# Kernel optimization log

Measured on AMD Instinct MI355X. Metric: run time of the kernel, lower is better.

The kernel has to match this reference:

```python
import jax, jax.numpy as jnp
import numpy as np
from math import ceil

WIDTH, HEIGHT, NUM_TILE = 1920, 1080, 16
# NOTE: original code computes BOTH block dims from height (bug preserved for faithfulness)
BLOCK_W = ceil(HEIGHT / NUM_TILE)
BLOCK_H = ceil(HEIGHT / NUM_TILE)
T = NUM_TILE * NUM_TILE  # 256 tiles
N = 65536


def setup_inputs() -> dict:
    key = jax.random.key(0)
    k1, k2, k3 = jax.random.split(key, 3)
    pos2d = jax.random.uniform(k1, (N, 2), jnp.float32) * jnp.array([WIDTH, HEIGHT], jnp.float32)
    radius = jax.random.uniform(k2, (N,), jnp.float32) * 2.0  # radius in tile units, avg ~3x3 tile footprint
    depth = jax.random.uniform(k3, (N,), jnp.float32) * 10.0
    return {"pos2d": pos2d, "radius": radius, "depth": depth}


def _tile_binning(pos2d, radius, depth):
    minval, maxval = 0.0, NUM_TILE - 1e-5
    xmin = jnp.clip(pos2d[:, 0] / BLOCK_W - radius, minval, maxval).astype(jnp.int32)
    xmax = jnp.clip(pos2d[:, 0] / BLOCK_W + radius, minval, maxval).astype(jnp.int32)
    ymin = jnp.clip(pos2d[:, 1] / BLOCK_H - radius, minval, maxval).astype(jnp.int32)
    ymax = jnp.clip(pos2d[:, 1] / BLOCK_H + radius, minval, maxval).astype(jnp.int32)

    tr = jnp.arange(NUM_TILE, dtype=jnp.int32)
    in_x = (tr[None, :] >= xmin[:, None]) & (tr[None, :] <= xmax[:, None])  # [N, 16]
    in_y = (tr[None, :] >= ymin[:, None]) & (tr[None, :] <= ymax[:, None])  # [N, 16]
    # tile index t = xi + NUM_TILE * yi  -> mask[n, yi, xi]
    mask = (in_y[:, :, None] & in_x[:, None, :]).reshape(N, T)  # [N, T]

    # inclusive-cumsum bucket offsets (matches torch.cumsum(tile_count))
    tile_count = jnp.cumsum(mask.sum(axis=0).astype(jnp.int32)).astype(jnp.int32)  # [T]
    total = tile_count[-1]

    # flattened entry list, tile-major then primitive-index order (matches scatter loop order)
    maskT = mask.T.reshape(-1)                                   # [T*N]
    tile_id = jnp.repeat(jnp.arange(T, dtype=jnp.int32), N)      # [T*N]
    prim_id = jnp.tile(jnp.arange(N, dtype=jnp.int32), T)        # [T*N]
    depth_e = depth[prim_id]
    tile_eff = jnp.where(maskT, tile_id, T)  # invalid entries pushed past all real tiles

    # segmented depth sort: primary key tile, secondary depth, tertiary prim (stable tiebreak)
    order = jnp.lexsort((prim_id, depth_e, tile_eff))
    prim_sorted = prim_id[order]
    valid = jnp.arange(T * N) < total
    tile_indices = jnp.where(valid, prim_sorted, -1).astype(jnp.int32)  # [T*N], -1 padded
    return tile_count, tile_indices


def reference(pos2d, radius, depth):
    # Equivalent of Screen.create_tiles(pos2d, radius) followed by Screen.depth_sort(depth).
    # Returns (tile_count: inclusive cumsum bucket offsets [T],
    #          tile_indices: per-tile depth-sorted primitive ids, padded to T*N with -1).
    return _tile_binning(pos2d, radius, depth)
```

## Files before the change

kernel.cpp:

```cpp
#include <hip/hip_runtime.h>
#include <stdint.h>

#define NPRIM 65536
#define NT 16
#define T_TILES 256
#define NBKT 2048
#define BCAP 256
#define NBLK 64
#define CTHR 512

typedef unsigned long long u64;
typedef unsigned int u32;

__device__ __forceinline__ u32 dbucket(float d) {
    u32 b = (u32)(d * 204.8f);
    return b > (NBKT - 1) ? (NBKT - 1) : b;
}

__global__ __launch_bounds__(256) void k_compute(
    const float2* __restrict__ pos2d, const float* __restrict__ radius,
    const float* __restrict__ depth, u64* __restrict__ keysRaw,
    u32* __restrict__ bounds, u32* __restrict__ counts_blk,
    u32* __restrict__ bh)
{
    __shared__ u32 hist[T_TILES];
    __shared__ u32 bhist[NBKT];
    int tid = threadIdx.x;
    hist[tid] = 0;
    for (int j = tid; j < NBKT; j += 256) bhist[j] = 0;
    __syncthreads();

    int base = blockIdx.x * 1024;
    const float mx = (float)(16.0 - 1e-5);
    #pragma unroll
    for (int q = 0; q < 4; ++q) {
        int i = base + q * 256 + tid;
        float2 p = pos2d[i];
        float r = radius[i];
        float fx = p.x / 68.0f;
        float fy = p.y / 68.0f;
        int xmin = (int)fminf(fmaxf(fx - r, 0.0f), mx);
        int xmax = (int)fminf(fmaxf(fx + r, 0.0f), mx);
        int ymin = (int)fminf(fmaxf(fy - r, 0.0f), mx);
        int ymax = (int)fminf(fmaxf(fy + r, 0.0f), mx);
        bounds[i] = (u32)(xmin | (xmax << 4) | (ymin << 8) | (ymax << 12));
        float d = depth[i];
        u32 lrank = atomicAdd(&bhist[dbucket(d)], 1u);
        keysRaw[i] = ((u64)lrank << 48) | ((u64)__float_as_uint(d) << 16) | (u32)i;
        for (int ty = ymin; ty <= ymax; ++ty)
            for (int tx = xmin; tx <= xmax; ++tx)
                atomicAdd(&hist[ty * NT + tx], 1u);
    }
    __syncthreads();
    counts_blk[blockIdx.x * 256 + tid] = hist[tid];
    for (int j = tid; j < NBKT; j += 256) bh[blockIdx.x * NBKT + j] = bhist[j];
}

__global__ __launch_bounds__(256) void k_scatter(
    const u64* __restrict__ keysRaw, const u32* __restrict__ bh,
    u64* __restrict__ keysBkt, u32* __restrict__ bucket_base,
    u32* __restrict__ bucket_count, const u32* __restrict__ counts_blk,
    int* __restrict__ tile_count, u32* __restrict__ excl_off)
{
    __shared__ u32 wsum[4];
    int tid = threadIdx.x, lane = tid & 63, wave = tid >> 6;
    int blk = blockIdx.x;

    if (blk == NBLK) {
        u32 s = 0;
        for (int bb = 0; bb < NBLK; ++bb) s += counts_blk[bb * 256 + tid];
        u32 v = s;
        #pragma unroll
        for (int d = 1; d < 64; d <<= 1) {
            u32 t = __shfl_up(v, d, 64);
            if (lane >= d) v += t;
        }
        if (lane == 63) wsum[wave] = v;
        __syncthreads();
        u32 add = 0;
        for (int w = 0; w < wave; ++w) add += wsum[w];
        u32 incl = v + add;
        tile_count[tid] = (int)incl;
        excl_off[tid] = incl - s;
        return;
    }

    __shared__ u32 loff[NBKT];
    u32 c8[8] = {0,0,0,0,0,0,0,0};
    u32 p8[8] = {0,0,0,0,0,0,0,0};
    for (int b = 0; b < NBLK; ++b) {
        const uint4* row = (const uint4*)(bh + b * NBKT + tid * 8);
        uint4 h0 = row[0], h1 = row[1];
        u32 h[8] = {h0.x, h0.y, h0.z, h0.w, h1.x, h1.y, h1.z, h1.w};
        #pragma unroll
        for (int j = 0; j < 8; ++j) {
            if (b < blk) p8[j] += h[j];
            c8[j] += h[j];
        }
    }
    u32 sum8 = 0;
    #pragma unroll
    for (int j = 0; j < 8; ++j) sum8 += c8[j];
    u32 v = sum8;
    #pragma unroll
    for (int d = 1; d < 64; d <<= 1) {
        u32 t = __shfl_up(v, d, 64);
        if (lane >= d) v += t;
    }
    if (lane == 63) wsum[wave] = v;
    __syncthreads();
    u32 add = 0;
    for (int w = 0; w < wave; ++w) add += wsum[w];
    u32 run = v + add - sum8;
    #pragma unroll
    for (int j = 0; j < 8; ++j) {
        loff[tid * 8 + j] = run + p8[j];
        if (blk == 0) {
            bucket_base[tid * 8 + j] = run;
            bucket_count[tid * 8 + j] = c8[j];
        }
        run += c8[j];
    }
    __syncthreads();

    int base = blk * 1024;
    #pragma unroll
    for (int q = 0; q < 4; ++q) {
        u64 key = keysRaw[base + q * 256 + tid];
        u32 d = dbucket(__uint_as_float((u32)(key >> 16)));
        u32 lrank = (u32)(key >> 48);
        keysBkt[loff[d] + lrank] = key & 0x0000FFFFFFFFFFFFull;
    }
}

__global__ __launch_bounds__(256) void k_bsort(
    const u64* __restrict__ keysBkt, const u32* __restrict__ bucket_base,
    const u32* __restrict__ bucket_count, const u32* __restrict__ bounds,
    u32* __restrict__ entries)
{
    __shared__ u64 buf[4][BCAP];
    int tid = threadIdx.x, lane = tid & 63, wave = tid >> 6;
    int bucket = blockIdx.x * 4 + wave;
    u32 base = bucket_base[bucket];
    u32 n = bucket_count[bucket];
    if (n > BCAP) n = BCAP;
    #pragma unroll
    for (int t = 0; t < 4; ++t) {
        u32 i = (u32)lane + 64u * t;
        if (i < n) buf[wave][i] = keysBkt[base + i];
    }
    __syncthreads();
    #pragma unroll
    for (int t = 0; t < 4; ++t) {
        u32 i = (u32)lane + 64u * t;
        if (i < n) {
            u64 ki = buf[wave][i];
            u32 r = 0;
            for (u32 j = 0; j < n; ++j) r += (buf[wave][j] < ki);
            u32 prim = (u32)ki & 0xFFFFu;
            entries[base + r] = (bounds[prim] << 16) | prim;
        }
    }
}

__global__ __launch_bounds__(CTHR) void k_compact(
    const uint4* __restrict__ entries4, const u32* __restrict__ excl_off,
    int* __restrict__ out_idx)
{
    __shared__ u32 chunkcnt[64];
    __shared__ u32 chunkoff[64];
    int tile = blockIdx.x, tid = threadIdx.x, lane = tid & 63, wave = tid >> 6;
    int tx = tile & 15, ty = tile >> 4;
    u32 base0 = excl_off[tile];
    u64 lmask = (1ull << lane) - 1;

    for (int cc = 0; cc < 8; ++cc) {
        int ch = wave * 8 + cc;
        u32 cs = 0;
        #pragma unroll
        for (int k = 0; k < 4; ++k) {
            uint4 e = entries4[ch * 256 + k * 64 + lane];
            u32 ev[4] = {e.x, e.y, e.z, e.w};
            #pragma unroll
            for (int q = 0; q < 4; ++q) {
                u32 bb2 = ev[q] >> 16;
                bool m = (tx >= (int)(bb2 & 15)) && (tx <= (int)((bb2 >> 4) & 15))
                      && (ty >= (int)((bb2 >> 8) & 15)) && (ty <= (int)((bb2 >> 12) & 15));
                cs += (u32)__popcll(__ballot(m));
            }
        }
        if (lane == 0) chunkcnt[ch] = cs;
    }
    __syncthreads();
    if (tid < 64) {
        u32 c2 = chunkcnt[tid], v2 = c2;
        #pragma unroll
        for (int d = 1; d < 64; d <<= 1) {
            u32 t = __shfl_up(v2, d, 64);
            if (lane >= d) v2 += t;
        }
        chunkoff[tid] = base0 + v2 - c2;
    }
    __syncthreads();

    for (int cc = 0; cc < 8; ++cc) {
        int ch = wave * 8 + cc;
        u32 run = chunkoff[ch];
        #pragma unroll
        for (int k = 0; k < 4; ++k) {
            uint4 e = entries4[ch * 256 + k * 64 + lane];
            u32 ev[4] = {e.x, e.y, e.z, e.w};
            bool m[4]; u64 bal[4];
            #pragma unroll
            for (int q = 0; q < 4; ++q) {
                u32 bb2 = ev[q] >> 16;
                m[q] = (tx >= (int)(bb2 & 15)) && (tx <= (int)((bb2 >> 4) & 15))
                    && (ty >= (int)((bb2 >> 8) & 15)) && (ty <= (int)((bb2 >> 12) & 15));
                bal[q] = __ballot(m[q]);
            }
            u32 pre = (u32)(__popcll(bal[0] & lmask) + __popcll(bal[1] & lmask)
                          + __popcll(bal[2] & lmask) + __popcll(bal[3] & lmask));
            #pragma unroll
            for (int q = 0; q < 4; ++q) {
                if (m[q]) { out_idx[run + pre] = (int)(ev[q] & 0xFFFFu); pre++; }
            }
            run += (u32)(__popcll(bal[0]) + __popcll(bal[1])
                       + __popcll(bal[2]) + __popcll(bal[3]));
        }
    }
}

extern "C" void kernel_launch(void* const* d_in, const int* in_sizes, int n_in,
                              void* d_out, int out_size, void* d_ws, size_t ws_size,
                              hipStream_t stream)
{
    const float2* pos2d  = (const float2*)d_in[0];
    const float*  radius = (const float*)d_in[1];
    const float*  depth  = (const float*)d_in[2];

    int* out32        = (int*)d_out;
    int* tile_count   = out32;
    int* tile_indices = out32 + T_TILES;

    char* ws = (char*)d_ws;
    u64* keysRaw      = (u64*)(ws);
    u64* keysBkt      = (u64*)(ws + 512 * 1024);
    u32* bounds       = (u32*)(ws + 1024 * 1024);
    u32* counts_blk   = (u32*)(ws + 1280 * 1024);
    u32* bh           = (u32*)(ws + 1344 * 1024);
    u32* bucket_base  = (u32*)(ws + 1856 * 1024);
    u32* bucket_count = (u32*)(ws + 1864 * 1024);
    u32* excl_off     = (u32*)(ws + 1872 * 1024);

    (void)hipMemsetAsync(tile_indices, 0xFF, (size_t)T_TILES * NPRIM * 4, stream);

    k_compute<<<NBLK, 256, 0, stream>>>(pos2d, radius, depth, keysRaw, bounds,
                                        counts_blk, bh);
    k_scatter<<<NBLK + 1, 256, 0, stream>>>(keysRaw, bh, keysBkt,
                                            bucket_base, bucket_count,
                                            counts_blk, tile_count, excl_off);

    u32* entries = (u32*)keysRaw;
    k_bsort<<<NBKT / 4, 256, 0, stream>>>(keysBkt, bucket_base, bucket_count,
                                          bounds, entries);
    k_compact<<<T_TILES, CTHR, 0, stream>>>((const uint4*)entries, excl_off,
                                            tile_indices);
}
```

Measured before the change: 150.1 us.

## Split bucket scan into single-block kernel and scatter via global atomic cursors

The per-block prefix over 64 block histograms that every scatter block used to recompute is replaced by one scan kernel. That kernel computes bucket bases and tile offsets once and seeds a global cursor array. Scatter then claims positions with global atomics instead of precomputed per-block local ranks, so the local-rank atomic and its key packing are dropped from the compute kernel. This removes redundant histogram reads but adds a kernel launch and global atomic contention. It also makes within-bucket order nondeterministic, which the later bucket sort must absorb.

Measured after the change: 146.4 us. 2.4% less time.

```diff
diff --git a/kernel.cpp b/kernel.cpp
--- a/kernel.cpp
+++ b/kernel.cpp
@@ -45,8 +45,8 @@
         int ymax = (int)fminf(fmaxf(fy + r, 0.0f), mx);
         bounds[i] = (u32)(xmin | (xmax << 4) | (ymin << 8) | (ymax << 12));
         float d = depth[i];
-        u32 lrank = atomicAdd(&bhist[dbucket(d)], 1u);
-        keysRaw[i] = ((u64)lrank << 48) | ((u64)__float_as_uint(d) << 16) | (u32)i;
+        keysRaw[i] = ((u64)__float_as_uint(d) << 16) | (u32)i;
+        atomicAdd(&bhist[dbucket(d)], 1u);
         for (int ty = ymin; ty <= ymax; ++ty)
             for (int tx = xmin; tx <= xmax; ++tx)
                 atomicAdd(&hist[ty * NT + tx], 1u);
@@ -56,51 +56,23 @@
     for (int j = tid; j < NBKT; j += 256) bh[blockIdx.x * NBKT + j] = bhist[j];
 }
 
-__global__ __launch_bounds__(256) void k_scatter(
-    const u64* __restrict__ keysRaw, const u32* __restrict__ bh,
-    u64* __restrict__ keysBkt, u32* __restrict__ bucket_base,
-    u32* __restrict__ bucket_count, const u32* __restrict__ counts_blk,
-    int* __restrict__ tile_count, u32* __restrict__ excl_off)
+__global__ __launch_bounds__(256) void k_scan(
+    const u32* __restrict__ bh, const u32* __restrict__ counts_blk,
+    u32* __restrict__ bucket_base, u32* __restrict__ bucket_count,
+    u32* __restrict__ cursor, int* __restrict__ tile_count,
+    u32* __restrict__ excl_off)
 {
     __shared__ u32 wsum[4];
     int tid = threadIdx.x, lane = tid & 63, wave = tid >> 6;
-    int blk = blockIdx.x;
-
-    if (blk == NBLK) {
-        u32 s = 0;
-        for (int bb = 0; bb < NBLK; ++bb) s += counts_blk[bb * 256 + tid];
-        u32 v = s;
-        #pragma unroll
-        for (int d = 1; d < 64; d <<= 1) {
-            u32 t = __shfl_up(v, d, 64);
-            if (lane >= d) v += t;
-        }
-        if (lane == 63) wsum[wave] = v;
-        __syncthreads();
-        u32 add = 0;
-        for (int w = 0; w < wave; ++w) add += wsum[w];
-        u32 incl = v + add;
-        tile_count[tid] = (int)incl;
-        excl_off[tid] = incl - s;
-        return;
-    }
-
-    __shared__ u32 loff[NBKT];
+
     u32 c8[8] = {0,0,0,0,0,0,0,0};
-    u32 p8[8] = {0,0,0,0,0,0,0,0};
     for (int b = 0; b < NBLK; ++b) {
         const uint4* row = (const uint4*)(bh + b * NBKT + tid * 8);
         uint4 h0 = row[0], h1 = row[1];
-        u32 h[8] = {h0.x, h0.y, h0.z, h0.w, h1.x, h1.y, h1.z, h1.w};
-        #pragma unroll
-        for (int j = 0; j < 8; ++j) {
-            if (b < blk) p8[j] += h[j];
-            c8[j] += h[j];
-        }
-    }
-    u32 sum8 = 0;
-    #pragma unroll
-    for (int j = 0; j < 8; ++j) sum8 += c8[j];
+        c8[0] += h0.x; c8[1] += h0.y; c8[2] += h0.z; c8[3] += h0.w;
+        c8[4] += h1.x; c8[5] += h1.y; c8[6] += h1.z; c8[7] += h1.w;
+    }
+    u32 sum8 = c8[0]+c8[1]+c8[2]+c8[3]+c8[4]+c8[5]+c8[6]+c8[7];
     u32 v = sum8;
     #pragma unroll
     for (int d = 1; d < 64; d <<= 1) {
@@ -114,22 +86,42 @@
     u32 run = v + add - sum8;
     #pragma unroll
     for (int j = 0; j < 8; ++j) {
-        loff[tid * 8 + j] = run + p8[j];
-        if (blk == 0) {
-            bucket_base[tid * 8 + j] = run;
-            bucket_count[tid * 8 + j] = c8[j];
-        }
+        bucket_base[tid * 8 + j] = run;
+        cursor[tid * 8 + j] = run;
+        bucket_count[tid * 8 + j] = c8[j];
         run += c8[j];
     }
     __syncthreads();
 
-    int base = blk * 1024;
+    u32 s = 0;
+    for (int bb = 0; bb < NBLK; ++bb) s += counts_blk[bb * 256 + tid];
+    v = s;
+    #pragma unroll
+    for (int d = 1; d < 64; d <<= 1) {
+        u32 t = __shfl_up(v, d, 64);
+        if (lane >= d) v += t;
+    }
+    if (lane == 63) wsum[wave] = v;
+    __syncthreads();
+    add = 0;
+    for (int w = 0; w < wave; ++w) add += wsum[w];
+    u32 incl = v + add;
+    tile_count[tid] = (int)incl;
+    excl_off[tid] = incl - s;
+}
+
+__global__ __launch_bounds__(256) void k_scatter(
+    const u64* __restrict__ keysRaw, u32* __restrict__ cursor,
+    u64* __restrict__ keysBkt)
+{
+    int base = blockIdx.x * 1024;
+    int tid = threadIdx.x;
     #pragma unroll
     for (int q = 0; q < 4; ++q) {
         u64 key = keysRaw[base + q * 256 + tid];
         u32 d = dbucket(__uint_as_float((u32)(key >> 16)));
-        u32 lrank = (u32)(key >> 48);
-        keysBkt[loff[d] + lrank] = key & 0x0000FFFFFFFFFFFFull;
+        u32 pos = atomicAdd(&cursor[d], 1u);
+        keysBkt[pos] = key;
     }
 }
 
@@ -250,15 +242,16 @@
     u32* bh           = (u32*)(ws + 1344 * 1024);
     u32* bucket_base  = (u32*)(ws + 1856 * 1024);
     u32* bucket_count = (u32*)(ws + 1864 * 1024);
-    u32* excl_off     = (u32*)(ws + 1872 * 1024);
+    u32* cursor       = (u32*)(ws + 1872 * 1024);
+    u32* excl_off     = (u32*)(ws + 1880 * 1024);
 
     (void)hipMemsetAsync(tile_indices, 0xFF, (size_t)T_TILES * NPRIM * 4, stream);
 
     k_compute<<<NBLK, 256, 0, stream>>>(pos2d, radius, depth, keysRaw, bounds,
                                         counts_blk, bh);
-    k_scatter<<<NBLK + 1, 256, 0, stream>>>(keysRaw, bh, keysBkt,
-                                            bucket_base, bucket_count,
-                                            counts_blk, tile_count, excl_off);
+    k_scan<<<1, 256, 0, stream>>>(bh, counts_blk, bucket_base, bucket_count,
+                                  cursor, tile_count, excl_off);
+    k_scatter<<<NBLK, 256, 0, stream>>>(keysRaw, cursor, keysBkt);
 
     u32* entries = (u32*)keysRaw;
     k_bsort<<<NBKT / 4, 256, 0, stream>>>(keysBkt, bucket_base, bucket_count,
```
